# Kernel optimization log

Measured on AMD Instinct MI355X. Metric: run time of the kernel, lower is better.

The kernel has to match this reference:

```python
import jax, jax.numpy as jnp
import numpy as np

N = 10000      # nodes
E = 160000     # edges
IN = 512       # in_feat
H = 512        # hidden_dim
L = 6          # layers
C = 64         # num_class
EPS = 1e-5     # BatchNorm eps


def setup_inputs() -> dict:
    key = jax.random.key(0)
    ks = jax.random.split(key, 12)
    x = jax.random.normal(ks[0], (N, IN), jnp.float32)
    src = jax.random.randint(ks[1], (E,), 0, N)
    dst = jax.random.randint(ks[2], (E,), 0, N)
    W0 = jax.random.normal(ks[3], (IN, H), jnp.float32) * (1.0 / np.sqrt(IN))
    Ws = jax.random.normal(ks[4], (L - 1, H, H), jnp.float32) * (1.0 / np.sqrt(H))
    bs = jnp.zeros((L, H), jnp.float32)
    gamma = jnp.ones((L, H), jnp.float32) + 0.1 * jax.random.normal(ks[5], (L, H), jnp.float32)
    beta = 0.1 * jax.random.normal(ks[6], (L, H), jnp.float32)
    run_mean = 0.1 * jax.random.normal(ks[7], (L, H), jnp.float32)
    run_var = jax.random.uniform(ks[8], (L, H), jnp.float32, 0.5, 1.5)
    linW = jax.random.normal(ks[9], (L * H, C), jnp.float32) * (1.0 / np.sqrt(L * H))
    linb = jnp.zeros((C,), jnp.float32)
    return {"x": x, "W0": W0, "Ws": Ws, "bs": bs, "gamma": gamma, "beta": beta,
            "run_mean": run_mean, "run_var": run_var, "linW": linW, "linb": linb,
            "src": src, "dst": dst}


def reference(x, W0, Ws, bs, gamma, beta, run_mean, run_var, linW, linb, src, dst):
    ones_e = jnp.ones((E,), jnp.float32)
    out_deg = jax.ops.segment_sum(ones_e, src, num_segments=N)
    in_deg = jax.ops.segment_sum(ones_e, dst, num_segments=N)
    # DGL GraphConv norm='both': D_dst^{-1/2} A D_src^{-1/2}, zero-deg clamped to 1
    norm_src = jnp.clip(out_deg, 1.0, None) ** -0.5   # [N]
    norm_dst = jnp.clip(in_deg, 1.0, None) ** -0.5    # [N]

    h = x
    hs = []
    for i in range(L):
        W = W0 if i == 0 else Ws[i - 1]
        m = (h * norm_src[:, None]) @ W                 # [N, H] GEMM
        agg = jax.ops.segment_sum(m[src], dst, num_segments=N)  # gather/scatter
        h = agg * norm_dst[:, None] + bs[i]
        # BatchNorm1d (inference, running stats) + ReLU; dropout is identity in eval
        scale = gamma[i] * jax.lax.rsqrt(run_var[i] + EPS)
        h = jax.nn.relu((h - run_mean[i]) * scale + beta[i])
        hs.append(h)
    h = jnp.concatenate(hs, axis=-1)                    # [N, L*H] JK-concat
    return h @ linW + linb                              # [N, C]
```

## Files before the change

### kernel.cpp

```cpp
#include <hip/hip_runtime.h>

#define NN 10000
#define NNPAD 10112
#define NE 160000
#define HF 512
#define LL 6
#define NC 64
#define KCAT (LL*HF)
#define BN_EPS 1e-5f
#define FSPLIT 3

typedef _Float16 f16x8 __attribute__((ext_vector_type(8)));
typedef _Float16 f16x4 __attribute__((ext_vector_type(4)));
typedef float f32x4 __attribute__((ext_vector_type(4)));

#define GLB(p) ((const __attribute__((address_space(1))) void*)(p))
#define LDSP(p) ((__attribute__((address_space(3))) void*)(p))


__global__ void zero_u32_kernel(unsigned* __restrict__ p, int n) {
  int i = blockIdx.x * blockDim.x + threadIdx.x;
  if (i < n) p[i] = 0u;
}

__global__ void deg_kernel(const int* __restrict__ src, const int* __restrict__ dst,
                           unsigned* __restrict__ cnt_out, unsigned* __restrict__ cnt_in) {
  int e = blockIdx.x * blockDim.x + threadIdx.x;
  if (e < NE) {
    atomicAdd(&cnt_out[src[e]], 1u);
    atomicAdd(&cnt_in[dst[e]], 1u);
  }
}

__global__ void prep_kernel(const unsigned* __restrict__ cnt_out, const unsigned* __restrict__ cnt_in,
                            float* __restrict__ norm_src, float* __restrict__ norm_dst,
                            const float* __restrict__ bs, const float* __restrict__ gamma,
                            const float* __restrict__ beta, const float* __restrict__ rmean,
                            const float* __restrict__ rvar,
                            float* __restrict__ scale, float* __restrict__ shift) {
  int i = blockIdx.x * blockDim.x + threadIdx.x;
  if (i < NN) {
    unsigned co = cnt_out[i]; if (co < 1u) co = 1u;
    unsigned ci = cnt_in[i];  if (ci < 1u) ci = 1u;
    norm_src[i] = rsqrtf((float)co);
    norm_dst[i] = rsqrtf((float)ci);
  }
  if (i < LL * HF) {
    float s = gamma[i] * rsqrtf(rvar[i] + BN_EPS);
    scale[i] = s;
    shift[i] = (bs[i] - rmean[i]) * s + beta[i];
  }
}

__global__ void scan_kernel(const unsigned* __restrict__ cnt, unsigned* __restrict__ off) {
  __shared__ unsigned wsum[16];
  int tid = threadIdx.x;
  int lane = tid & 63, wid = tid >> 6;
  unsigned base = 0;
  for (int c = 0; c < NN; c += 1024) {
    int i = c + tid;
    unsigned v = (i < NN) ? cnt[i] : 0u;
    unsigned x = v;
    #pragma unroll
    for (int d = 1; d < 64; d <<= 1) {
      unsigned y = __shfl_up(x, d, 64);
      if (lane >= d) x += y;
    }
    if (lane == 63) wsum[wid] = x;
    __syncthreads();
    if (wid == 0 && lane < 16) {
      unsigned s = wsum[lane];
      #pragma unroll
      for (int d = 1; d < 16; d <<= 1) {
        unsigned y = __shfl_up(s, d, 16);
        if (lane >= d) s += y;
      }
      wsum[lane] = s;
    }
    __syncthreads();
    unsigned wbase = wid ? wsum[wid - 1] : 0u;
    if (i < NN) off[i] = base + wbase + x - v;
    unsigned tot = wsum[15];
    __syncthreads();
    base += tot;
  }
  if (tid == 0) off[NN] = base;
}

__global__ void fill_kernel(const int* __restrict__ src, const int* __restrict__ dst,
                            const unsigned* __restrict__ off, unsigned* __restrict__ cursor,
                            int* __restrict__ edge_src) {
  int e = blockIdx.x * blockDim.x + threadIdx.x;
  if (e < NE) {
    int d = dst[e];
    unsigned p = atomicAdd(&cursor[d], 1u);
    edge_src[off[d] + p] = src[e];
  }
}

__global__ void convert_w(const float* __restrict__ W0, const float* __restrict__ Ws,
                          _Float16* __restrict__ Wt) {
  int l = blockIdx.z;
  const float* W = (l == 0) ? W0 : (Ws + (size_t)(l - 1) * HF * HF);
  __shared__ float t[32][33];
  int n0 = blockIdx.x * 32, k0 = blockIdx.y * 32;
  int tx = threadIdx.x & 31, ty4 = (threadIdx.x >> 5) * 4;
  #pragma unroll
  for (int j = 0; j < 4; ++j)
    t[ty4 + j][tx] = W[(size_t)(k0 + ty4 + j) * HF + n0 + tx];
  __syncthreads();
  size_t base = (size_t)l * HF * HF;
  #pragma unroll
  for (int j = 0; j < 4; ++j)
    Wt[base + (size_t)(n0 + ty4 + j) * HF + k0 + tx] = (_Float16)t[tx][ty4 + j];
}

__global__ void convert_lin(const float* __restrict__ linW, _Float16* __restrict__ Lt) {
  __shared__ float t[32][33];
  int n0 = blockIdx.x * 32, k0 = blockIdx.y * 32;
  int tx = threadIdx.x & 31, ty4 = (threadIdx.x >> 5) * 4;
  #pragma unroll
  for (int j = 0; j < 4; ++j)
    t[ty4 + j][tx] = linW[(size_t)(k0 + ty4 + j) * NC + n0 + tx];
  __syncthreads();
  #pragma unroll
  for (int j = 0; j < 4; ++j)
    Lt[(size_t)(n0 + ty4 + j) * KCAT + k0 + tx] = (_Float16)t[tx][ty4 + j];
}

__global__ void split_x(const float* __restrict__ x, _Float16* __restrict__ zh) {
  int i = blockIdx.x * blockDim.x + threadIdx.x;
  if (i >= NN * HF / 4) return;
  int base = i * 4;
  float4 v = *(const float4*)&x[base];
  f16x4 h;
  h.x = (_Float16)v.x;
  h.y = (_Float16)v.y;
  h.z = (_Float16)v.z;
  h.w = (_Float16)v.w;
  *(f16x4*)&zh[base] = h;
}

__launch_bounds__(256, 2)
__global__ void gemm_layer_f16(const _Float16* __restrict__ Z, int lda,
                               const _Float16* __restrict__ Wt,
                               const float* __restrict__ nsrc,
                               _Float16* __restrict__ Mout) {
  __shared__ _Float16 As[128][64];
  __shared__ _Float16 Bs[128][64];
  int m0 = blockIdx.y * 128;
  int n0 = blockIdx.x * 128;
  int wid = threadIdx.x >> 6, lane = threadIdx.x & 63;
  int wr = wid >> 1, wc = wid & 1;
  int fr = lane & 15, kg = lane >> 4;
  int rr = lane >> 3;
  int ck = (lane & 7) ^ rr;

  f32x4 acc[4][4];
  #pragma unroll
  for (int m = 0; m < 4; ++m)
    #pragma unroll
    for (int n = 0; n < 4; ++n)
      acc[m][n] = (f32x4){0.f, 0.f, 0.f, 0.f};

  const _Float16* gA = Z  + (size_t)(m0 + wid * 32 + rr) * lda + ck * 8;
  const _Float16* gB = Wt + (size_t)(n0 + wid * 32 + rr) * HF + ck * 8;

  for (int k0 = 0; k0 < HF; k0 += 64) {
    __syncthreads();
    #pragma unroll
    for (int i = 0; i < 4; ++i) {
      __builtin_amdgcn_global_load_lds(GLB(gA + (size_t)i * 8 * lda + k0),
                                       LDSP(&As[wid * 32 + i * 8][0]), 16, 0, 0);
      __builtin_amdgcn_global_load_lds(GLB(gB + (size_t)i * 8 * HF + k0),
                                       LDSP(&Bs[wid * 32 + i * 8][0]), 16, 0, 0);
    }
    __syncthreads();
    #pragma unroll
    for (int kk = 0; kk < 2; ++kk) {
      f16x8 a[4], b[4];
      #pragma unroll
      for (int n = 0; n < 4; ++n) {
        int row = wc * 64 + n * 16 + fr;
        b[n] = *(const f16x8*)&Bs[row][((kk * 4 + kg) ^ (row & 7)) * 8];
      }
      #pragma unroll
      for (int m = 0; m < 4; ++m) {
        int row = wr * 64 + m * 16 + fr;
        a[m] = *(const f16x8*)&As[row][((kk * 4 + kg) ^ (row & 7)) * 8];
      }
      #pragma unroll
      for (int m = 0; m < 4; ++m)
        #pragma unroll
        for (int n = 0; n < 4; ++n)
          acc[m][n] = __builtin_amdgcn_mfma_f32_16x16x32_f16(a[m], b[n], acc[m][n], 0, 0, 0);
    }
  }
  #pragma unroll
  for (int m = 0; m < 4; ++m) {
    #pragma unroll
    for (int j = 0; j < 4; ++j) {
      int row = m0 + wr * 64 + m * 16 + kg * 4 + j;
      if (row < NN) {
        float s = nsrc[row];
        #pragma unroll
        for (int n = 0; n < 4; ++n) {
          int col = n0 + wc * 64 + n * 16 + fr;
          Mout[(size_t)row * HF + col] = (_Float16)(acc[m][n][j] * s);
        }
      }
    }
  }
}

__launch_bounds__(256)
__global__ void agg_bn_kernel(const _Float16* __restrict__ Mm,
                              const int* __restrict__ edge_src,
                              const unsigned* __restrict__ row_off,
                              const float* __restrict__ norm_dst,
                              const float* __restrict__ bn_scale,
                              const float* __restrict__ bn_shift,
                              _Float16* __restrict__ hcat_col) {
  int s     = blockIdx.x & 7;
  int chunk = s >> 1;
  int grp   = blockIdx.x >> 3;
  int wave  = threadIdx.x >> 6;
  int sub   = (threadIdx.x >> 4) & 3;
  int n = grp * 32 + (s & 1) * 16 + wave * 4 + sub;
  if (n >= NN) return;
  int f = chunk * 128 + (threadIdx.x & 15) * 8;
  unsigned e0 = row_off[n], e1 = row_off[n + 1];
  float a0=0.f,a1=0.f,a2=0.f,a3=0.f,a4=0.f,a5=0.f,a6=0.f,a7=0.f;
  unsigned e = e0;
  for (; e + 4 <= e1; e += 4) {
    int s0 = edge_src[e], s1 = edge_src[e + 1], s2 = edge_src[e + 2], s3 = edge_src[e + 3];
    f16x8 v0 = *(const f16x8*)&Mm[(size_t)s0 * HF + f];
    f16x8 v1 = *(const f16x8*)&Mm[(size_t)s1 * HF + f];
    f16x8 v2 = *(const f16x8*)&Mm[(size_t)s2 * HF + f];
    f16x8 v3 = *(const f16x8*)&Mm[(size_t)s3 * HF + f];
    a0 += (float)v0[0]+(float)v1[0]+(float)v2[0]+(float)v3[0];
    a1 += (float)v0[1]+(float)v1[1]+(float)v2[1]+(float)v3[1];
    a2 += (float)v0[2]+(float)v1[2]+(float)v2[2]+(float)v3[2];
    a3 += (float)v0[3]+(float)v1[3]+(float)v2[3]+(float)v3[3];
    a4 += (float)v0[4]+(float)v1[4]+(float)v2[4]+(float)v3[4];
    a5 += (float)v0[5]+(float)v1[5]+(float)v2[5]+(float)v3[5];
    a6 += (float)v0[6]+(float)v1[6]+(float)v2[6]+(float)v3[6];
    a7 += (float)v0[7]+(float)v1[7]+(float)v2[7]+(float)v3[7];
  }
  for (; e < e1; ++e) {
    int sx = edge_src[e];
    f16x8 v = *(const f16x8*)&Mm[(size_t)sx * HF + f];
    a0 += (float)v[0]; a1 += (float)v[1]; a2 += (float)v[2]; a3 += (float)v[3];
    a4 += (float)v[4]; a5 += (float)v[5]; a6 += (float)v[6]; a7 += (float)v[7];
  }
  float nd = norm_dst[n];
  float4 s0 = *(const float4*)&bn_scale[f];
  float4 s1 = *(const float4*)&bn_scale[f + 4];
  float4 t0 = *(const float4*)&bn_shift[f];
  float4 t1 = *(const float4*)&bn_shift[f + 4];
  float y0 = fmaxf(fmaf(a0 * nd, s0.x, t0.x), 0.f);
  float y1 = fmaxf(fmaf(a1 * nd, s0.y, t0.y), 0.f);
  float y2 = fmaxf(fmaf(a2 * nd, s0.z, t0.z), 0.f);
  float y3 = fmaxf(fmaf(a3 * nd, s0.w, t0.w), 0.f);
  float y4 = fmaxf(fmaf(a4 * nd, s1.x, t1.x), 0.f);
  float y5 = fmaxf(fmaf(a5 * nd, s1.y, t1.y), 0.f);
  float y6 = fmaxf(fmaf(a6 * nd, s1.z, t1.z), 0.f);
  float y7 = fmaxf(fmaf(a7 * nd, s1.w, t1.w), 0.f);
  f16x8 hv;
  hv[0]=(_Float16)y0; hv[1]=(_Float16)y1; hv[2]=(_Float16)y2; hv[3]=(_Float16)y3;
  hv[4]=(_Float16)y4; hv[5]=(_Float16)y5; hv[6]=(_Float16)y6; hv[7]=(_Float16)y7;
  *(f16x8*)&hcat_col[(size_t)n * KCAT + f] = hv;
}

__launch_bounds__(256, 2)
__global__ void final_gemm_f16(const _Float16* __restrict__ Hc,
                               const _Float16* __restrict__ Lt,
                               float* __restrict__ part) {
  __shared__ _Float16 As[128][64];
  __shared__ _Float16 Bs[64][64];
  int m0 = blockIdx.x * 128;
  int sp = blockIdx.y;
  int kbase = sp * (KCAT / FSPLIT);
  int wid = threadIdx.x >> 6, lane = threadIdx.x & 63;
  int fr = lane & 15, kg = lane >> 4;
  int rr = lane >> 3;
  int ck = (lane & 7) ^ rr;

  f32x4 acc[2][4];
  #pragma unroll
  for (int m = 0; m < 2; ++m)
    #pragma unroll
    for (int n = 0; n < 4; ++n)
      acc[m][n] = (f32x4){0.f, 0.f, 0.f, 0.f};

  const _Float16* gA = Hc + (size_t)(m0 + wid * 32 + rr) * KCAT + kbase + ck * 8;
  const _Float16* gB = Lt + (size_t)(wid * 16 + rr) * KCAT + kbase + ck * 8;

  for (int k0 = 0; k0 < KCAT / FSPLIT; k0 += 64) {
    __syncthreads();
    #pragma unroll
    for (int i = 0; i < 4; ++i)
      __builtin_amdgcn_global_load_lds(GLB(gA + (size_t)i * 8 * KCAT + k0),
                                       LDSP(&As[wid * 32 + i * 8][0]), 16, 0, 0);
    #pragma unroll
    for (int i = 0; i < 2; ++i)
      __builtin_amdgcn_global_load_lds(GLB(gB + (size_t)i * 8 * KCAT + k0),
                                       LDSP(&Bs[wid * 16 + i * 8][0]), 16, 0, 0);
    __syncthreads();
    #pragma unroll
    for (int kk = 0; kk < 2; ++kk) {
      f16x8 a[2], b[4];
      #pragma unroll
      for (int n = 0; n < 4; ++n) {
        int row = n * 16 + fr;
        b[n] = *(const f16x8*)&Bs[row][((kk * 4 + kg) ^ (row & 7)) * 8];
      }
      #pragma unroll
      for (int m = 0; m < 2; ++m) {
        int row = wid * 32 + m * 16 + fr;
        a[m] = *(const f16x8*)&As[row][((kk * 4 + kg) ^ (row & 7)) * 8];
      }
      #pragma unroll
      for (int m = 0; m < 2; ++m)
        #pragma unroll
        for (int n = 0; n < 4; ++n)
          acc[m][n] = __builtin_amdgcn_mfma_f32_16x16x32_f16(a[m], b[n], acc[m][n], 0, 0, 0);
    }
  }
  #pragma unroll
  for (int m = 0; m < 2; ++m) {
    #pragma unroll
    for (int j = 0; j < 4; ++j) {
      int row = m0 + wid * 32 + m * 16 + kg * 4 + j;
      if (row < NN) {
        #pragma unroll
        for (int n = 0; n < 4; ++n) {
          int col = n * 16 + fr;
          part[((size_t)sp * NN + row) * NC + col] = acc[m][n][j];
        }
      }
    }
  }
}

__launch_bounds__(256)
__global__ void final_reduce(const float* __restrict__ part,
                             const float* __restrict__ linb,
                             float* __restrict__ out) {
  int i = blockIdx.x * blockDim.x + threadIdx.x;
  if (i >= NN * NC / 4) return;
  int n  = i >> 4;
  int cq = i & 15;
  float4 s = *(const float4*)&linb[cq * 4];
  #pragma unroll
  for (int sp = 0; sp < FSPLIT; ++sp) {
    float4 v = *(const float4*)&part[((size_t)sp * NN + n) * NC + cq * 4];
    s.x += v.x; s.y += v.y; s.z += v.z; s.w += v.w;
  }
  *(float4*)&out[(size_t)n * NC + cq * 4] = s;
}


extern "C" void kernel_launch(void* const* d_in, const int* in_sizes, int n_in,
                              void* d_out, int out_size, void* d_ws, size_t ws_size,
                              hipStream_t stream) {
  const float* x     = (const float*)d_in[0];
  const float* W0    = (const float*)d_in[1];
  const float* Ws    = (const float*)d_in[2];
  const float* bs    = (const float*)d_in[3];
  const float* gamma = (const float*)d_in[4];
  const float* beta  = (const float*)d_in[5];
  const float* rmean = (const float*)d_in[6];
  const float* rvar  = (const float*)d_in[7];
  const float* linW  = (const float*)d_in[8];
  const float* linb  = (const float*)d_in[9];
  const int*   src   = (const int*)d_in[10];
  const int*   dst   = (const int*)d_in[11];
  float* out = (float*)d_out;

  char* w = (char*)d_ws;
  size_t o = 0;
  auto carve = [&](size_t bytes) -> void* {
    o = (o + 255) & ~(size_t)255;
    void* p = w + o;
    o += bytes;
    return p;
  };
  _Float16*  m_buf = (_Float16*)carve((size_t)NNPAD * HF * 2);
  _Float16*  hcat  = (_Float16*)carve((size_t)NNPAD * KCAT * 2);
  _Float16*  zh    = (_Float16*)carve((size_t)NNPAD * HF * 2);
  _Float16*  wt    = (_Float16*)carve((size_t)LL * HF * HF * 2);
  _Float16*  lt    = (_Float16*)carve((size_t)NC * KCAT * 2);
  float*     part  = (float*)carve((size_t)FSPLIT * NN * NC * 4);
  float*     bnsc  = (float*)carve((size_t)LL * HF * 4);
  float*     bnsh  = (float*)carve((size_t)LL * HF * 4);
  float*     nsrc  = (float*)carve((size_t)NN * 4);
  float*     ndst  = (float*)carve((size_t)NN * 4);
  unsigned*  cnts  = (unsigned*)carve((size_t)3 * NN * 4);
  unsigned*  roff  = (unsigned*)carve((size_t)(NN + 1) * 4);
  int*       esrc  = (int*)carve((size_t)NE * 4);

  unsigned* cnt_out = cnts;
  unsigned* cnt_in  = cnts + NN;
  unsigned* cursor  = cnts + 2 * NN;

  zero_u32_kernel<<<(3 * NN + 255) / 256, 256, 0, stream>>>(cnts, 3 * NN);
  deg_kernel<<<(NE + 255) / 256, 256, 0, stream>>>(src, dst, cnt_out, cnt_in);
  prep_kernel<<<(NN + 255) / 256, 256, 0, stream>>>(cnt_out, cnt_in, nsrc, ndst,
                                                    bs, gamma, beta, rmean, rvar, bnsc, bnsh);
  scan_kernel<<<1, 1024, 0, stream>>>(cnt_in, roff);
  fill_kernel<<<(NE + 255) / 256, 256, 0, stream>>>(src, dst, roff, cursor, esrc);
  convert_w<<<dim3(16, 16, 6), 256, 0, stream>>>(W0, Ws, wt);
  convert_lin<<<dim3(2, 96), 256, 0, stream>>>(linW, lt);
  split_x<<<(NN * HF / 4 + 255) / 256, 256, 0, stream>>>(x, zh);

  int agg_blocks = ((NN + 31) / 32) * 8;
  for (int l = 0; l < LL; ++l) {
    const _Float16* A   = (l == 0) ? zh : (hcat + (size_t)(l - 1) * HF);
    int             lda = (l == 0) ? HF : KCAT;
    gemm_layer_f16<<<dim3(HF / 128, NNPAD / 128), 256, 0, stream>>>(
        A, lda, wt + (size_t)l * HF * HF, nsrc, m_buf);
    agg_bn_kernel<<<agg_blocks, 256, 0, stream>>>(m_buf, esrc, roff, ndst,
                                                  bnsc + l * HF, bnsh + l * HF,
                                                  hcat + (size_t)l * HF);
  }
  final_gemm_f16<<<dim3(NNPAD / 128, FSPLIT), 256, 0, stream>>>(hcat, lt, part);
  final_reduce<<<(NN * NC / 4 + 255) / 256, 256, 0, stream>>>(part, linb, out);
}
```

Measured before the change: 276.9 us.

## Fuse entire GNN pipeline into one persistent cooperative kernel with grid syncs

Replaces the sequence of roughly twenty kernel launches with a single cooperative persistent kernel that uses grid-wide barriers between stages: preprocessing, CSR build, per-layer GEMM and aggregation, final GEMM and reduction. The aim is to remove launch gaps and tail effects between the many short kernels. The tradeoffs are that the grid is capped at the co-resident block count, so GEMM and aggregation tiles are processed in persistent loops. Each grid.sync also adds its own cost, and the original multi-kernel path is kept as a fallback if the cooperative launch fails.

After: 989.2 us. +257.3%, slower.

```diff
diff --git a/kernel.cpp b/kernel.cpp
--- a/kernel.cpp
+++ b/kernel.cpp
@@ -1,4 +1,7 @@
 #include <hip/hip_runtime.h>
+#include <hip/hip_cooperative_groups.h>
+
+namespace cg = cooperative_groups;
 
 #define NN 10000
 #define NNPAD 10112
@@ -9,6 +12,9 @@
 #define KCAT (LL*HF)
 #define BN_EPS 1e-5f
 #define FSPLIT 3
+#define AGG_SLOTS (((NN + 31) / 32) * 8)
+#define GEMM_TILES 316
+#define FIN_TILES (79 * FSPLIT)
 
 typedef _Float16 f16x8 __attribute__((ext_vector_type(8)));
 typedef _Float16 f16x4 __attribute__((ext_vector_type(4)));
@@ -16,6 +22,329 @@
 
 #define GLB(p) ((const __attribute__((address_space(1))) void*)(p))
 #define LDSP(p) ((__attribute__((address_space(3))) void*)(p))
+
+struct Params {
+  const float* x; const float* W0; const float* Ws; const float* bs;
+  const float* gamma; const float* beta; const float* rmean; const float* rvar;
+  const float* linW; const float* linb; const int* src; const int* dst;
+  float* out;
+  _Float16* m_buf; _Float16* hcat; _Float16* zh; _Float16* wt; _Float16* lt;
+  float* part; float* bnsc; float* bnsh; float* nsrc; float* ndst;
+  unsigned* cnts; unsigned* roff; int* esrc;
+};
+
+__launch_bounds__(256, 2)
+__global__ void mono_kernel(Params p) {
+  cg::grid_group grid = cg::this_grid();
+  __shared__ __align__(16) char lds[32768];
+  _Float16 (*As)[64] = reinterpret_cast<_Float16 (*)[64]>(lds);
+  _Float16 (*Bs)[64] = reinterpret_cast<_Float16 (*)[64]>(lds + 16384);
+  float (*t32)[33]   = reinterpret_cast<float (*)[33]>(lds);
+  unsigned* wsum     = reinterpret_cast<unsigned*>(lds);
+
+  const int tid  = threadIdx.x;
+  const int bid  = blockIdx.x;
+  const int nblk = gridDim.x;
+  const int gsz  = nblk * 256;
+  const int gtid = bid * 256 + tid;
+
+  for (int i = gtid; i < 3 * NN; i += gsz) p.cnts[i] = 0u;
+  for (int i = gtid; i < NN * HF / 4; i += gsz) {
+    float4 v = *(const float4*)&p.x[i * 4];
+    f16x4 h; h.x = (_Float16)v.x; h.y = (_Float16)v.y; h.z = (_Float16)v.z; h.w = (_Float16)v.w;
+    *(f16x4*)&p.zh[i * 4] = h;
+  }
+  {
+    int tx = tid & 31, ty4 = (tid >> 5) * 4;
+    for (int t = bid; t < 1536 + 192; t += nblk) {
+      __syncthreads();
+      if (t < 1536) {
+        int l = t / 256, r = t % 256;
+        int n0 = (r & 15) * 32, k0 = (r >> 4) * 32;
+        const float* W = (l == 0) ? p.W0 : (p.Ws + (size_t)(l - 1) * HF * HF);
+        #pragma unroll
+        for (int j = 0; j < 4; ++j)
+          t32[ty4 + j][tx] = W[(size_t)(k0 + ty4 + j) * HF + n0 + tx];
+        __syncthreads();
+        size_t base = (size_t)l * HF * HF;
+        #pragma unroll
+        for (int j = 0; j < 4; ++j)
+          p.wt[base + (size_t)(n0 + ty4 + j) * HF + k0 + tx] = (_Float16)t32[tx][ty4 + j];
+      } else {
+        int r = t - 1536;
+        int n0 = (r & 1) * 32, k0 = (r >> 1) * 32;
+        #pragma unroll
+        for (int j = 0; j < 4; ++j)
+          t32[ty4 + j][tx] = p.linW[(size_t)(k0 + ty4 + j) * NC + n0 + tx];
+        __syncthreads();
+        #pragma unroll
+        for (int j = 0; j < 4; ++j)
+          p.lt[(size_t)(n0 + ty4 + j) * KCAT + k0 + tx] = (_Float16)t32[tx][ty4 + j];
+      }
+    }
+  }
+  grid.sync();
+
+  for (int e = gtid; e < NE; e += gsz) {
+    atomicAdd(&p.cnts[p.src[e]], 1u);
+    atomicAdd(&p.cnts[NN + p.dst[e]], 1u);
+  }
+  grid.sync();
+
+  if (bid == 0) {
+    const unsigned* cnt = p.cnts + NN;
+    int lane = tid & 63, wv = tid >> 6;
+    unsigned base = 0;
+    for (int c = 0; c < NN; c += 256) {
+      int i = c + tid;
+      unsigned v = (i < NN) ? cnt[i] : 0u;
+      unsigned x = v;
+      #pragma unroll
+      for (int d = 1; d < 64; d <<= 1) {
+        unsigned y = __shfl_up(x, d, 64);
+        if (lane >= d) x += y;
+      }
+      if (lane == 63) wsum[wv] = x;
+      __syncthreads();
+      if (tid == 0) {
+        unsigned s = 0;
+        #pragma unroll
+        for (int j = 0; j < 4; ++j) { s += wsum[j]; wsum[j] = s; }
+      }
+      __syncthreads();
+      unsigned wbase = wv ? wsum[wv - 1] : 0u;
+      if (i < NN) p.roff[i] = base + wbase + x - v;
+      unsigned tot = wsum[3];
+      __syncthreads();
+      base += tot;
+    }
+    if (tid == 0) p.roff[NN] = base;
+  } else {
+    for (int i = (bid - 1) * 256 + tid; i < NN; i += (nblk - 1) * 256) {
+      unsigned co = p.cnts[i];      if (co < 1u) co = 1u;
+      unsigned ci = p.cnts[NN + i]; if (ci < 1u) ci = 1u;
+      p.nsrc[i] = rsqrtf((float)co);
+      p.ndst[i] = rsqrtf((float)ci);
+      if (i < LL * HF) {
+        float s = p.gamma[i] * rsqrtf(p.rvar[i] + BN_EPS);
+        p.bnsc[i] = s;
+        p.bnsh[i] = (p.bs[i] - p.rmean[i]) * s + p.beta[i];
+      }
+    }
+  }
+  grid.sync();
+
+  for (int e = gtid; e < NE; e += gsz) {
+    int d = p.dst[e];
+    unsigned pos = atomicAdd(&p.cnts[2 * NN + d], 1u);
+    p.esrc[p.roff[d] + pos] = p.src[e];
+  }
+  grid.sync();
+
+  const int wid = tid >> 6, lane = tid & 63;
+  const int wr = wid >> 1, wc = wid & 1;
+  const int fr = lane & 15, kg = lane >> 4;
+  const int rr = lane >> 3;
+  const int ck = (lane & 7) ^ rr;
+
+  for (int l = 0; l < LL; ++l) {
+    const _Float16* __restrict__ Z = (l == 0) ? p.zh : (p.hcat + (size_t)(l - 1) * HF);
+    int lda = (l == 0) ? HF : KCAT;
+    const _Float16* __restrict__ Wt = p.wt + (size_t)l * HF * HF;
+
+    for (int t = bid; t < GEMM_TILES; t += nblk) {
+      int m0 = (t >> 2) * 128;
+      int n0 = (t & 3) * 128;
+      f32x4 acc[4][4];
+      #pragma unroll
+      for (int m = 0; m < 4; ++m)
+        #pragma unroll
+        for (int n = 0; n < 4; ++n)
+          acc[m][n] = (f32x4){0.f, 0.f, 0.f, 0.f};
+
+      const _Float16* gA = Z  + (size_t)(m0 + wid * 32 + rr) * lda + ck * 8;
+      const _Float16* gB = Wt + (size_t)(n0 + wid * 32 + rr) * HF + ck * 8;
+
+      for (int k0 = 0; k0 < HF; k0 += 64) {
+        __syncthreads();
+        #pragma unroll
+        for (int i = 0; i < 4; ++i) {
+          __builtin_amdgcn_global_load_lds(GLB(gA + (size_t)i * 8 * lda + k0),
+                                           LDSP(&As[wid * 32 + i * 8][0]), 16, 0, 0);
+          __builtin_amdgcn_global_load_lds(GLB(gB + (size_t)i * 8 * HF + k0),
+                                           LDSP(&Bs[wid * 32 + i * 8][0]), 16, 0, 0);
+        }
+        __syncthreads();
+        #pragma unroll
+        for (int kk = 0; kk < 2; ++kk) {
+          f16x8 a[4], b[4];
+          #pragma unroll
+          for (int n = 0; n < 4; ++n) {
+            int row = wc * 64 + n * 16 + fr;
+            b[n] = *(const f16x8*)&Bs[row][((kk * 4 + kg) ^ (row & 7)) * 8];
+          }
+          #pragma unroll
+          for (int m = 0; m < 4; ++m) {
+            int row = wr * 64 + m * 16 + fr;
+            a[m] = *(const f16x8*)&As[row][((kk * 4 + kg) ^ (row & 7)) * 8];
+          }
+          #pragma unroll
+          for (int m = 0; m < 4; ++m)
+            #pragma unroll
+            for (int n = 0; n < 4; ++n)
+              acc[m][n] = __builtin_amdgcn_mfma_f32_16x16x32_f16(a[m], b[n], acc[m][n], 0, 0, 0);
+        }
+      }
+      #pragma unroll
+      for (int m = 0; m < 4; ++m) {
+        #pragma unroll
+        for (int j = 0; j < 4; ++j) {
+          int row = m0 + wr * 64 + m * 16 + kg * 4 + j;
+          if (row < NN) {
+            float s = p.nsrc[row];
+            #pragma unroll
+            for (int n = 0; n < 4; ++n) {
+              int col = n0 + wc * 64 + n * 16 + fr;
+              p.m_buf[(size_t)row * HF + col] = (_Float16)(acc[m][n][j] * s);
+            }
+          }
+        }
+      }
+      __syncthreads();
+    }
+    grid.sync();
+
+    {
+      const float* __restrict__ bnsc = p.bnsc + l * HF;
+      const float* __restrict__ bnsh = p.bnsh + l * HF;
+      _Float16* __restrict__ hc = p.hcat + (size_t)l * HF;
+      for (int b = bid; b < AGG_SLOTS; b += nblk) {
+        int sl = b & 7, chunk = sl >> 1, grp = b >> 3;
+        int wave = tid >> 6, sub = (tid >> 4) & 3;
+        int n = grp * 32 + (sl & 1) * 16 + wave * 4 + sub;
+        if (n < NN) {
+          int f = chunk * 128 + (tid & 15) * 8;
+          unsigned e0 = p.roff[n], e1 = p.roff[n + 1];
+          float a0=0.f,a1=0.f,a2=0.f,a3=0.f,a4=0.f,a5=0.f,a6=0.f,a7=0.f;
+          unsigned e = e0;
+          for (; e + 4 <= e1; e += 4) {
+            int es0 = p.esrc[e], es1 = p.esrc[e+1], es2 = p.esrc[e+2], es3 = p.esrc[e+3];
+            f16x8 v0 = *(const f16x8*)&p.m_buf[(size_t)es0 * HF + f];
+            f16x8 v1 = *(const f16x8*)&p.m_buf[(size_t)es1 * HF + f];
+            f16x8 v2 = *(const f16x8*)&p.m_buf[(size_t)es2 * HF + f];
+            f16x8 v3 = *(const f16x8*)&p.m_buf[(size_t)es3 * HF + f];
+            a0 += (float)v0[0]+(float)v1[0]+(float)v2[0]+(float)v3[0];
+            a1 += (float)v0[1]+(float)v1[1]+(float)v2[1]+(float)v3[1];
+            a2 += (float)v0[2]+(float)v1[2]+(float)v2[2]+(float)v3[2];
+            a3 += (float)v0[3]+(float)v1[3]+(float)v2[3]+(float)v3[3];
+            a4 += (float)v0[4]+(float)v1[4]+(float)v2[4]+(float)v3[4];
+            a5 += (float)v0[5]+(float)v1[5]+(float)v2[5]+(float)v3[5];
+            a6 += (float)v0[6]+(float)v1[6]+(float)v2[6]+(float)v3[6];
+            a7 += (float)v0[7]+(float)v1[7]+(float)v2[7]+(float)v3[7];
+          }
+          for (; e < e1; ++e) {
+            int es = p.esrc[e];
+            f16x8 v = *(const f16x8*)&p.m_buf[(size_t)es * HF + f];
+            a0 += (float)v[0]; a1 += (float)v[1]; a2 += (float)v[2]; a3 += (float)v[3];
+            a4 += (float)v[4]; a5 += (float)v[5]; a6 += (float)v[6]; a7 += (float)v[7];
+          }
+          float nd = p.ndst[n];
+          float4 sc0 = *(const float4*)&bnsc[f];
+          float4 sc1 = *(const float4*)&bnsc[f + 4];
+          float4 sh0 = *(const float4*)&bnsh[f];
+          float4 sh1 = *(const float4*)&bnsh[f + 4];
+          float y0 = fmaxf(fmaf(a0 * nd, sc0.x, sh0.x), 0.f);
+          float y1 = fmaxf(fmaf(a1 * nd, sc0.y, sh0.y), 0.f);
+          float y2 = fmaxf(fmaf(a2 * nd, sc0.z, sh0.z), 0.f);
+          float y3 = fmaxf(fmaf(a3 * nd, sc0.w, sh0.w), 0.f);
+          float y4 = fmaxf(fmaf(a4 * nd, sc1.x, sh1.x), 0.f);
+          float y5 = fmaxf(fmaf(a5 * nd, sc1.y, sh1.y), 0.f);
+          float y6 = fmaxf(fmaf(a6 * nd, sc1.z, sh1.z), 0.f);
+          float y7 = fmaxf(fmaf(a7 * nd, sc1.w, sh1.w), 0.f);
+          f16x8 hv;
+          hv[0]=(_Float16)y0; hv[1]=(_Float16)y1; hv[2]=(_Float16)y2; hv[3]=(_Float16)y3;
+          hv[4]=(_Float16)y4; hv[5]=(_Float16)y5; hv[6]=(_Float16)y6; hv[7]=(_Float16)y7;
+          *(f16x8*)&hc[(size_t)n * KCAT + f] = hv;
+        }
+      }
+    }
+    grid.sync();
+  }
+
+  for (int t = bid; t < FIN_TILES; t += nblk) {
+    int m0 = (t % 79) * 128;
+    int sp = t / 79;
+    int kbase = sp * (KCAT / FSPLIT);
+    f32x4 acc[2][4];
+    #pragma unroll
+    for (int m = 0; m < 2; ++m)
+      #pragma unroll
+      for (int n = 0; n < 4; ++n)
+        acc[m][n] = (f32x4){0.f, 0.f, 0.f, 0.f};
+
+    const _Float16* gA = p.hcat + (size_t)(m0 + wid * 32 + rr) * KCAT + kbase + ck * 8;
+    const _Float16* gB = p.lt   + (size_t)(wid * 16 + rr) * KCAT + kbase + ck * 8;
+
+    for (int k0 = 0; k0 < KCAT / FSPLIT; k0 += 64) {
+      __syncthreads();
+      #pragma unroll
+      for (int i = 0; i < 4; ++i)
+        __builtin_amdgcn_global_load_lds(GLB(gA + (size_t)i * 8 * KCAT + k0),
+                                         LDSP(&As[wid * 32 + i * 8][0]), 16, 0, 0);
+      #pragma unroll
+      for (int i = 0; i < 2; ++i)
+        __builtin_amdgcn_global_load_lds(GLB(gB + (size_t)i * 8 * KCAT + k0),
+                                         LDSP(&Bs[wid * 16 + i * 8][0]), 16, 0, 0);
+      __syncthreads();
+      #pragma unroll
+      for (int kk = 0; kk < 2; ++kk) {
+        f16x8 a[2], b[4];
+        #pragma unroll
+        for (int n = 0; n < 4; ++n) {
+          int row = n * 16 + fr;
+          b[n] = *(const f16x8*)&Bs[row][((kk * 4 + kg) ^ (row & 7)) * 8];
+        }
+        #pragma unroll
+        for (int m = 0; m < 2; ++m) {
+          int row = wid * 32 + m * 16 + fr;
+          a[m] = *(const f16x8*)&As[row][((kk * 4 + kg) ^ (row & 7)) * 8];
+        }
+        #pragma unroll
+        for (int m = 0; m < 2; ++m)
+          #pragma unroll
+          for (int n = 0; n < 4; ++n)
+            acc[m][n] = __builtin_amdgcn_mfma_f32_16x16x32_f16(a[m], b[n], acc[m][n], 0, 0, 0);
+      }
+    }
+    #pragma unroll
+    for (int m = 0; m < 2; ++m) {
+      #pragma unroll
+      for (int j = 0; j < 4; ++j) {
+        int row = m0 + wid * 32 + m * 16 + kg * 4 + j;
+        if (row < NN) {
+          #pragma unroll
+          for (int n = 0; n < 4; ++n) {
+            int col = n * 16 + fr;
+            p.part[((size_t)sp * NN + row) * NC + col] = acc[m][n][j];
+          }
+        }
+      }
+    }
+    __syncthreads();
+  }
+  grid.sync();
+
+  for (int i = gtid; i < NN * NC / 4; i += gsz) {
+    int n = i >> 4, cq = i & 15;
+    float4 s = *(const float4*)&p.linb[cq * 4];
+    #pragma unroll
+    for (int sp = 0; sp < FSPLIT; ++sp) {
+      float4 v = *(const float4*)&p.part[((size_t)sp * NN + n) * NC + cq * 4];
+      s.x += v.x; s.y += v.y; s.z += v.z; s.w += v.w;
+    }
+    *(float4*)&p.out[(size_t)n * NC + cq * 4] = s;
+  }
+}
 
 
 __global__ void zero_u32_kernel(unsigned* __restrict__ p, int n) {
@@ -134,10 +463,7 @@
   int base = i * 4;
   float4 v = *(const float4*)&x[base];
   f16x4 h;
-  h.x = (_Float16)v.x;
-  h.y = (_Float16)v.y;
-  h.z = (_Float16)v.z;
-  h.w = (_Float16)v.w;
+  h.x = (_Float16)v.x; h.y = (_Float16)v.y; h.z = (_Float16)v.z; h.w = (_Float16)v.w;
   *(f16x4*)&zh[base] = h;
 }
 
@@ -364,66 +690,86 @@
 extern "C" void kernel_launch(void* const* d_in, const int* in_sizes, int n_in,
                               void* d_out, int out_size, void* d_ws, size_t ws_size,
                               hipStream_t stream) {
-  const float* x     = (const float*)d_in[0];
-  const float* W0    = (const float*)d_in[1];
-  const float* Ws    = (const float*)d_in[2];
-  const float* bs    = (const float*)d_in[3];
-  const float* gamma = (const float*)d_in[4];
-  const float* beta  = (const float*)d_in[5];
-  const float* rmean = (const float*)d_in[6];
-  const float* rvar  = (const float*)d_in[7];
-  const float* linW  = (const float*)d_in[8];
-  const float* linb  = (const float*)d_in[9];
-  const int*   src   = (const int*)d_in[10];
-  const int*   dst   = (const int*)d_in[11];
-  float* out = (float*)d_out;
-
   char* w = (char*)d_ws;
   size_t o = 0;
   auto carve = [&](size_t bytes) -> void* {
     o = (o + 255) & ~(size_t)255;
-    void* p = w + o;
+    void* ptr = w + o;
     o += bytes;
-    return p;
+    return ptr;
   };
-  _Float16*  m_buf = (_Float16*)carve((size_t)NNPAD * HF * 2);
-  _Float16*  hcat  = (_Float16*)carve((size_t)NNPAD * KCAT * 2);
-  _Float16*  zh    = (_Float16*)carve((size_t)NNPAD * HF * 2);
-  _Float16*  wt    = (_Float16*)carve((size_t)LL * HF * HF * 2);
-  _Float16*  lt    = (_Float16*)carve((size_t)NC * KCAT * 2);
-  float*     part  = (float*)carve((size_t)FSPLIT * NN * NC * 4);
-  float*     bnsc  = (float*)carve((size_t)LL * HF * 4);
-  float*     bnsh  = (float*)carve((size_t)LL * HF * 4);
-  float*     nsrc  = (float*)carve((size_t)NN * 4);
-  float*     ndst  = (float*)carve((size_t)NN * 4);
-  unsigned*  cnts  = (unsigned*)carve((size_t)3 * NN * 4);
-  unsigned*  roff  = (unsigned*)carve((size_t)(NN + 1) * 4);
-  int*       esrc  = (int*)carve((size_t)NE * 4);
-
-  unsigned* cnt_out = cnts;
-  unsigned* cnt_in  = cnts + NN;
-  unsigned* cursor  = cnts + 2 * NN;
-
-  zero_u32_kernel<<<(3 * NN + 255) / 256, 256, 0, stream>>>(cnts, 3 * NN);
-  deg_kernel<<<(NE + 255) / 256, 256, 0, stream>>>(src, dst, cnt_out, cnt_in);
-  prep_kernel<<<(NN + 255) / 256, 256, 0, stream>>>(cnt_out, cnt_in, nsrc, ndst,
-                                                    bs, gamma, beta, rmean, rvar, bnsc, bnsh);
-  scan_kernel<<<1, 1024, 0, stream>>>(cnt_in, roff);
-  fill_kernel<<<(NE + 255) / 256, 256, 0, stream>>>(src, dst, roff, cursor, esrc);
-  convert_w<<<dim3(16, 16, 6), 256, 0, stream>>>(W0, Ws, wt);
-  convert_lin<<<dim3(2, 96), 256, 0, stream>>>(linW, lt);
-  split_x<<<(NN * HF / 4 + 255) / 256, 256, 0, stream>>>(x, zh);
-
-  int agg_blocks = ((NN + 31) / 32) * 8;
+  Params p;
+  p.x     = (const float*)d_in[0];
+  p.W0    = (const float*)d_in[1];
+  p.Ws    = (const float*)d_in[2];
+  p.bs    = (const float*)d_in[3];
+  p.gamma = (const float*)d_in[4];
+  p.beta  = (const float*)d_in[5];
+  p.rmean = (const float*)d_in[6];
+  p.rvar  = (const float*)d_in[7];
+  p.linW  = (const float*)d_in[8];
+  p.linb  = (const float*)d_in[9];
+  p.src   = (const int*)d_in[10];
+  p.dst   = (const int*)d_in[11];
+  p.out   = (float*)d_out;
+
+  p.m_buf = (_Float16*)carve((size_t)NNPAD * HF * 2);
+  p.hcat  = (_Float16*)carve((size_t)NNPAD * KCAT * 2);
+  p.zh    = (_Float16*)carve((size_t)NNPAD * HF * 2);
+  p.wt    = (_Float16*)carve((size_t)LL * HF * HF * 2);
+  p.lt    = (_Float16*)carve((size_t)NC * KCAT * 2);
+  p.part  = (float*)carve((size_t)FSPLIT * NN * NC * 4);
+  p.bnsc  = (float*)carve((size_t)LL * HF * 4);
+  p.bnsh  = (float*)carve((size_t)LL * HF * 4);
+  p.nsrc  = (float*)carve((size_t)NN * 4);
+  p.ndst  = (float*)carve((size_t)NN * 4);
+  p.cnts  = (unsigned*)carve((size_t)3 * NN * 4);
+  p.roff  = (unsigned*)carve((size_t)(NN + 1) * 4);
+  p.esrc  = (int*)carve((size_t)NE * 4);
+
+  bool coop_ok = false;
+  int maxPerCU = 0, numCU = 0, dev = 0;
+  hipError_t e1 = hipGetDevice(&dev);
+  hipError_t e2 = hipDeviceGetAttribute(&numCU, hipDeviceAttributeMultiprocessorCount, dev);
+  hipError_t e3 = hipOccupancyMaxActiveBlocksPerMultiprocessor(
+      &maxPerCU, (const void*)mono_kernel, 256, 0);
+  if (e1 == hipSuccess && e2 == hipSuccess && e3 == hipSuccess && maxPerCU > 0 && numCU > 0) {
+    long grid = (long)maxPerCU * numCU;
+    if (grid > 1024) grid = 1024;
+    grid = (grid / 8) * 8;
+    if (grid >= 8) {
+      void* args[] = { &p };
+      hipError_t el = hipLaunchCooperativeKernel((void*)mono_kernel,
+                                                 dim3((unsigned)grid), dim3(256), args, 0, stream);
+      coop_ok = (el == hipSuccess);
+    }
+  }
+  if (coop_ok) return;
+
+  unsigned* cnt_out = p.cnts;
+  unsigned* cnt_in  = p.cnts + NN;
+  float* out = p.out;
+
+  zero_u32_kernel<<<(3 * NN + 255) / 256, 256, 0, stream>>>(p.cnts, 3 * NN);
+  deg_kernel<<<(NE + 255) / 256, 256, 0, stream>>>(p.src, p.dst, cnt_out, cnt_in);
+  prep_kernel<<<(NN + 255) / 256, 256, 0, stream>>>(cnt_out, cnt_in, p.nsrc, p.ndst,
+                                                    p.bs, p.gamma, p.beta, p.rmean, p.rvar,
+                                                    p.bnsc, p.bnsh);
+  scan_kernel<<<1, 1024, 0, stream>>>(cnt_in, p.roff);
+  fill_kernel<<<(NE + 255) / 256, 256, 0, stream>>>(p.src, p.dst, p.roff, p.cnts + 2 * NN, p.esrc);
+  convert_w<<<dim3(16, 16, 6), 256, 0, stream>>>(p.W0, p.Ws, p.wt);
+  convert_lin<<<dim3(2, 96), 256, 0, stream>>>(p.linW, p.lt);
+  split_x<<<(NN * HF / 4 + 255) / 256, 256, 0, stream>>>(p.x, p.zh);
+
   for (int l = 0; l < LL; ++l) {
-    const _Float16* A   = (l == 0) ? zh : (hcat + (size_t)(l - 1) * HF);
+    const _Float16* A   = (l == 0) ? p.zh : (p.hcat + (size_t)(l - 1) * HF);
     int             lda = (l == 0) ? HF : KCAT;
     gemm_layer_f16<<<dim3(HF / 128, NNPAD / 128), 256, 0, stream>>>(
-        A, lda, wt + (size_t)l * HF * HF, nsrc, m_buf);
-    agg_bn_kernel<<<agg_blocks, 256, 0, stream>>>(m_buf, esrc, roff, ndst,
-                                                  bnsc + l * HF, bnsh + l * HF,
-                                                  hcat + (size_t)l * HF);
-  }
-  final_gemm_f16<<<dim3(NNPAD / 128, FSPLIT), 256, 0, stream>>>(hcat, lt, part);
-  final_reduce<<<(NN * NC / 4 + 255) / 256, 256, 0, stream>>>(part, linb, out);
-}
+        A, lda, p.wt + (size_t)l * HF * HF, p.nsrc, p.m_buf);
+    agg_bn_kernel<<<AGG_SLOTS, 256, 0, stream>>>(p.m_buf, p.esrc, p.roff, p.ndst,
+                                                 p.bnsc + l * HF, p.bnsh + l * HF,
+                                                 p.hcat + (size_t)l * HF);
+  }
+  final_gemm_f16<<<dim3(NNPAD / 128, FSPLIT), 256, 0, stream>>>(p.hcat, p.lt, p.part);
+  final_reduce<<<(NN * NC / 4 + 255) / 256, 256, 0, stream>>>(p.part, p.linb, out);
+}
```
